# Optimization experiments

Hardware: AMD Instinct MI355X
Metric: run time of the kernel (lower is better)

Reference implementation:

```python
import jax, jax.numpy as jnp
import numpy as np
import math

HIDDEN = 1024
N_HEAD = 16
D_K = HIDDEN // N_HEAD

def setup_inputs() -> dict:
    key = jax.random.key(0)
    ks = jax.random.split(key, 6)
    B, T = 2, 2048
    x = jax.random.normal(ks[0], (B, T, HIDDEN), dtype=jnp.float32)
    mask = jax.random.randint(ks[1], (B, 1, 1, T), 0, 2, dtype=jnp.int32)
    s = 1.0 / math.sqrt(HIDDEN)
    W_qkv = jax.random.normal(ks[2], (HIDDEN, 3 * HIDDEN), dtype=jnp.float32) * s
    b_qkv = jnp.zeros((3 * HIDDEN,), dtype=jnp.float32)
    W_out = jax.random.normal(ks[3], (HIDDEN, HIDDEN), dtype=jnp.float32) * s
    b_out = jnp.zeros((HIDDEN,), dtype=jnp.float32)
    return {"x": x, "mask": mask, "W_qkv": W_qkv, "b_qkv": b_qkv, "W_out": W_out, "b_out": b_out}

def reference(x, mask, W_qkv, b_qkv, W_out, b_out):
    B, T, H = x.shape
    qkv = x @ W_qkv + b_qkv  # [B,T,3H]
    q, k, v = jnp.split(qkv, 3, axis=-1)
    # [B,T,H] -> [B,nh,T,dk]
    def split_heads(t):
        return t.reshape(B, T, N_HEAD, D_K).transpose(0, 2, 1, 3)
    q, k, v = split_heads(q), split_heads(k), split_heads(v)
    scores = jnp.einsum('bhqd,bhkd->bhqk', q, k) / math.sqrt(D_K)
    scores = jnp.where(mask == 0, jnp.float32(-1e9), scores)
    attn = jax.nn.softmax(scores, axis=-1)
    out = jnp.einsum('bhqk,bhkd->bhqd', attn, v)
    out = out.transpose(0, 2, 1, 3).reshape(B, T, H)
    return out @ W_out + b_out
```

## Files before the change

### kernel.cpp

```cpp
#include <hip/hip_runtime.h>
#include <stdint.h>

typedef unsigned short u16;
typedef unsigned int u32;
typedef short bf16x8 __attribute__((ext_vector_type(8)));
typedef float f32x4 __attribute__((ext_vector_type(4)));

#define MFMA16(a, b, c) __builtin_amdgcn_mfma_f32_16x16x32_bf16((a), (b), (c), 0, 0, 0)
#define BAR()                              \
  do {                                     \
    __builtin_amdgcn_sched_barrier(0);     \
    __builtin_amdgcn_s_barrier();          \
    __builtin_amdgcn_sched_barrier(0);     \
  } while (0)

__device__ __forceinline__ u16 f2bf(float f) {
  union { float f; u32 u; } v; v.f = f;
  u32 u = v.u;
  u32 r = (u + 0x7FFFu + ((u >> 16) & 1u)) >> 16;
  return (u16)r;
}
__device__ __forceinline__ float bf2f(u16 h) {
  union { u32 u; float f; } v; v.u = ((u32)h) << 16;
  return v.f;
}
__device__ __forceinline__ u32 cvtpk_bf16(float lo, float hi) {
  u32 r;
  asm("v_cvt_pk_bf16_f32 %0, %1, %2" : "=v"(r) : "v"(lo), "v"(hi));
  return r;
}

__device__ __forceinline__ void gload_lds16(const void* g, void* l) {
  __builtin_amdgcn_global_load_lds(
      (const __attribute__((address_space(1))) unsigned int*)g,
      (__attribute__((address_space(3))) unsigned int*)l,
      16, 0, 0);
}

__global__ __launch_bounds__(256) void transpose_weights(
    const float* __restrict__ Wqkv, u16* __restrict__ WtQ,
    const float* __restrict__ Wout, u16* __restrict__ WtO) {
  __shared__ u16 t[32][33];
  int id = blockIdx.x;
  const float* src;
  u16* dst;
  int C, bx, by;
  if (id < 3072) {
    src = Wqkv; dst = WtQ; C = 3072;
    bx = (id % 96) * 32; by = (id / 96) * 32;
  } else {
    id -= 3072;
    src = Wout; dst = WtO; C = 1024;
    bx = (id % 32) * 32; by = (id / 32) * 32;
  }
  const int R = 1024;
  const int tx = threadIdx.x & 31, ty = threadIdx.x >> 5;
#pragma unroll
  for (int i = 0; i < 32; i += 8)
    t[ty + i][tx] = f2bf(src[(size_t)(by + ty + i) * C + bx + tx]);
  __syncthreads();
#pragma unroll
  for (int i = 0; i < 32; i += 8)
    dst[(size_t)(bx + ty + i) * R + by + tx] = t[tx][ty + i];
}

__global__ __launch_bounds__(512) void mask_compact(
    const int* __restrict__ mask, int* __restrict__ idx, int* __restrict__ cnt) {
  const int b = blockIdx.x;
  const int tid = threadIdx.x;
  const int lane = tid & 63, wave = tid >> 6;
  __shared__ int wtot[8];
  int m[4], c = 0;
#pragma unroll
  for (int j = 0; j < 4; ++j) {
    m[j] = (mask[b * 2048 + tid * 4 + j] != 0);
    c += m[j];
  }
  int pfx = c;
#pragma unroll
  for (int sh = 1; sh < 64; sh <<= 1) {
    int v = __shfl_up(pfx, sh);
    if (lane >= sh) pfx += v;
  }
  if (lane == 63) wtot[wave] = pfx;
  int epfx = pfx - c;
  __syncthreads();
  int wbase = 0, total = 0;
#pragma unroll
  for (int w = 0; w < 8; ++w) {
    int v = wtot[w];
    if (w < wave) wbase += v;
    total += v;
  }
  int pos = b * 2048 + wbase + epfx;
#pragma unroll
  for (int j = 0; j < 4; ++j)
    if (m[j]) idx[pos++] = tid * 4 + j;
  for (int i = total + tid; i < 2048; i += 512) idx[b * 2048 + i] = 0;
  if (tid == 0) cnt[b] = total;
}

__global__ __launch_bounds__(256) void gemm_a32_bf16(
    const float* __restrict__ A, const u16* __restrict__ Bt,
    const float* __restrict__ bias, u16* __restrict__ Cout,
    int M, int N, int K) {
  __shared__ __align__(16) u16 As[128 * 64];
  __shared__ __align__(16) u16 Bs[2][128 * 64];
  const int tid = threadIdx.x;
  const int lane = tid & 63;
  const int wave = tid >> 6;
  const int nwg = gridDim.x;
  const int id = blockIdx.x;
  const int sw = (id & 7) * (nwg >> 3) + (id >> 3);
  const int nx = N >> 7;
  const int m0 = (sw / nx) * 128;
  const int n0 = (sw % nx) * 128;
  const int wm = (wave >> 1) * 64;
  const int wn = (wave & 1) * 64;

  f32x4 acc[4][4] = {};
  const char* Bbase = (const char*)Bt;
  float4 fa[4], fb[4];

#define A32_ISSUE_B(ktile, buf)                                                \
  _Pragma("unroll") for (int i = 0; i < 4; ++i) {                              \
    int flat = wave * 1024 + lane * 16 + i * 4096;                             \
    int row = flat >> 7;                                                       \
    int cb = flat & 127;                                                       \
    int scb = cb ^ ((row & 7) << 4);                                           \
    gload_lds16(Bbase + ((size_t)(n0 + row) * K + (ktile)) * 2 + scb,          \
                (char*)&Bs[buf][0] + flat);                                    \
  }

#define A32_LOAD_A(ktile)                                                      \
  _Pragma("unroll") for (int i = 0; i < 4; ++i) {                              \
    int flat = wave * 1024 + lane * 16 + i * 4096;                             \
    int row = flat >> 7;                                                       \
    int cb = flat & 127;                                                       \
    const float* ax = A + (size_t)(m0 + row) * K + (ktile) + (cb >> 1);        \
    fa[i] = *(const float4*)ax;                                                \
    fb[i] = *(const float4*)(ax + 4);                                          \
  }

#define A32_CVT()                                                              \
  _Pragma("unroll") for (int i = 0; i < 4; ++i) {                              \
    int flat = wave * 1024 + lane * 16 + i * 4096;                             \
    int row = flat >> 7;                                                       \
    int cb = flat & 127;                                                       \
    union { u32 w[4]; bf16x8 v; } o;                                           \
    o.w[0] = cvtpk_bf16(fa[i].x, fa[i].y);                                     \
    o.w[1] = cvtpk_bf16(fa[i].z, fa[i].w);                                     \
    o.w[2] = cvtpk_bf16(fb[i].x, fb[i].y);                                     \
    o.w[3] = cvtpk_bf16(fb[i].z, fb[i].w);                                     \
    *(bf16x8*)((char*)&As[0] + row * 128 + (cb ^ ((row & 7) << 4))) = o.v;     \
  }

  A32_ISSUE_B(0, 0);
  A32_LOAD_A(0);
  A32_CVT();
  asm volatile("s_waitcnt lgkmcnt(0)" ::: "memory");
  BAR();

  const int nsteps = K >> 6;
  for (int t = 0; t < nsteps; ++t) {
    if (t < nsteps - 1) {
      A32_ISSUE_B((t << 6) + 64, (t & 1) ^ 1);
      A32_LOAD_A((t << 6) + 64);
    }
    __builtin_amdgcn_sched_barrier(0);
#pragma unroll
    for (int ks = 0; ks < 2; ++ks) {
      const int col = (lane >> 4) * 8 + ks * 32;
      bf16x8 af[4], bfr[4];
#pragma unroll
      for (int mt = 0; mt < 4; ++mt) {
        int row = wm + mt * 16 + (lane & 15);
        af[mt] = *(const bf16x8*)((const char*)&As[0] + row * 128 +
                                  ((col * 2) ^ ((row & 7) << 4)));
      }
#pragma unroll
      for (int nt = 0; nt < 4; ++nt) {
        int row = wn + nt * 16 + (lane & 15);
        bfr[nt] = *(const bf16x8*)((const char*)&Bs[t & 1][0] + row * 128 +
                                   ((col * 2) ^ ((row & 7) << 4)));
      }
#pragma unroll
      for (int mt = 0; mt < 4; ++mt)
#pragma unroll
        for (int nt = 0; nt < 4; ++nt)
          acc[mt][nt] = MFMA16(af[mt], bfr[nt], acc[mt][nt]);
    }
    __builtin_amdgcn_sched_barrier(0);
    if (t < nsteps - 1) {
      BAR();
      A32_CVT();
      asm volatile("s_waitcnt lgkmcnt(0)" ::: "memory");
      BAR();
    }
  }
#undef A32_ISSUE_B
#undef A32_LOAD_A
#undef A32_CVT

  float bv[4];
#pragma unroll
  for (int nt = 0; nt < 4; ++nt)
    bv[nt] = bias[n0 + wn + nt * 16 + (lane & 15)];
#pragma unroll
  for (int mt = 0; mt < 4; ++mt)
#pragma unroll
    for (int nt = 0; nt < 4; ++nt)
#pragma unroll
      for (int r = 0; r < 4; ++r) {
        int m = m0 + wm + mt * 16 + (lane >> 4) * 4 + r;
        int n = n0 + wn + nt * 16 + (lane & 15);
        Cout[(size_t)m * N + n] = f2bf(acc[mt][nt][r] + bv[nt]);
      }
}

template <bool OUT_BF16>
__global__ __launch_bounds__(256) void gemm_bf16(
    const u16* __restrict__ A, const u16* __restrict__ Bt,
    const float* __restrict__ bias, void* __restrict__ Cout,
    int M, int N, int K) {
  __shared__ __align__(16) u16 As[2][128 * 64];
  __shared__ __align__(16) u16 Bs[2][128 * 64];
  const int tid = threadIdx.x;
  const int lane = tid & 63;
  const int wave = tid >> 6;
  const int nwg = gridDim.x;
  const int id = blockIdx.x;
  const int sw = (id & 7) * (nwg >> 3) + (id >> 3);
  const int nx = N >> 7;
  const int m0 = (sw / nx) * 128;
  const int n0 = (sw % nx) * 128;
  const int wm = (wave >> 1) * 64;
  const int wn = (wave & 1) * 64;

  f32x4 acc[4][4] = {};

  const char* Abase = (const char*)A;
  const char* Bbase = (const char*)Bt;

#define STAGE_AB(ktile, buf)                                                   \
  _Pragma("unroll") for (int i = 0; i < 4; ++i) {                              \
    int flat = wave * 1024 + lane * 16 + i * 4096;                             \
    int row = flat >> 7;                                                       \
    int cb = flat & 127;                                                       \
    int scb = cb ^ ((row & 7) << 4);                                           \
    gload_lds16(Abase + ((size_t)(m0 + row) * K + (ktile)) * 2 + scb,          \
                (char*)&As[buf][0] + flat);                                    \
    gload_lds16(Bbase + ((size_t)(n0 + row) * K + (ktile)) * 2 + scb,          \
                (char*)&Bs[buf][0] + flat);                                    \
  }

  STAGE_AB(0, 0);

  const int nsteps = K >> 6;
  for (int t = 0; t < nsteps; ++t) {
    asm volatile("s_waitcnt vmcnt(0)" ::: "memory");
    BAR();
    if (t < nsteps - 1) STAGE_AB((t << 6) + 64, (t & 1) ^ 1);
#pragma unroll
    for (int ks = 0; ks < 2; ++ks) {
      const int col = (lane >> 4) * 8 + ks * 32;
      bf16x8 af[4], bfr[4];
#pragma unroll
      for (int mt = 0; mt < 4; ++mt) {
        int row = wm + mt * 16 + (lane & 15);
        af[mt] = *(const bf16x8*)((const char*)&As[t & 1][0] + row * 128 +
                                  ((col * 2) ^ ((row & 7) << 4)));
      }
#pragma unroll
      for (int nt = 0; nt < 4; ++nt) {
        int row = wn + nt * 16 + (lane & 15);
        bfr[nt] = *(const bf16x8*)((const char*)&Bs[t & 1][0] + row * 128 +
                                   ((col * 2) ^ ((row & 7) << 4)));
      }
#pragma unroll
      for (int mt = 0; mt < 4; ++mt)
#pragma unroll
        for (int nt = 0; nt < 4; ++nt)
          acc[mt][nt] = MFMA16(af[mt], bfr[nt], acc[mt][nt]);
    }
  }
#undef STAGE_AB

  float bv[4];
#pragma unroll
  for (int nt = 0; nt < 4; ++nt)
    bv[nt] = bias[n0 + wn + nt * 16 + (lane & 15)];
#pragma unroll
  for (int mt = 0; mt < 4; ++mt)
#pragma unroll
    for (int nt = 0; nt < 4; ++nt)
#pragma unroll
      for (int r = 0; r < 4; ++r) {
        int m = m0 + wm + mt * 16 + (lane >> 4) * 4 + r;
        int n = n0 + wn + nt * 16 + (lane & 15);
        float v = acc[mt][nt][r] + bv[nt];
        if (OUT_BF16)
          ((u16*)Cout)[(size_t)m * N + n] = f2bf(v);
        else
          ((float*)Cout)[(size_t)m * N + n] = v;
      }
}

#define T_SEQ 2048
#define ROWQKV 3072
#define SCL 0.180336880f

template <bool SPLIT>
__global__ __launch_bounds__(512) void attn_fwd(
    const u16* __restrict__ qkv, const int* __restrict__ idx,
    const int* __restrict__ cnt, u16* __restrict__ outp,
    float* __restrict__ Ml) {
  __shared__ __align__(16) u16 Ks[2][2][64 * 64];
  __shared__ __align__(16) u16 Vt[2][2][64 * 64];
  __shared__ __align__(16) u32 lut[256 * 4];

  const int tid = threadIdx.x;
  const int lane = tid & 63;
  const int wave = tid >> 6;
  const int r15 = lane & 15;
  const int g = lane >> 4;
  const int id = blockIdx.x;
  const int hz = ((id >> 6) << 3) | (id & 7);
  const int qb = (id >> 3) & 7;
  const int h = SPLIT ? (hz >> 2) : (hz >> 1);
  const int z = SPLIT ? (hz & 3) : (hz & 1);
  const int split = SPLIT ? (z >> 1) : 0;
  const int b = SPLIT ? (z & 1) : z;
  const int q0 = qb * 256 + wave * 32;
  const size_t rowb = (size_t)b * T_SEQ;
  const int* idxb = idx + b * 2048;
  const int count = cnt[b];
  const int ntot = (count + 127) >> 7;
  const int nth = (ntot + 1) >> 1;
  const int t0 = (SPLIT && split) ? nth : 0;
  const int nt2 = SPLIT ? (split ? ntot - nth : nth) : ntot;

  const int Lk = wave * 1024 + lane * 16;
  const int krow = Lk >> 7;
  const int kscb = (Lk & 127) ^ ((krow & 7) << 4);
  const int kprow = ((krow >> 4) & 1) * 32 + ((krow >> 2) & 3) * 8 +
                    (krow >> 5) * 4 + (krow & 3);
  const int vkey = tid >> 3;
  const int vd0 = (tid & 7) * 8;

  for (int i = tid; i < 256; i += 512) {
    union { u32 w[4]; bf16x8 v; } e;
#pragma unroll
    for (int j = 0; j < 4; ++j)
      e.w[j] = (((i >> (2 * j)) & 1) ? 0x3F80u : 0u) |
               (((i >> (2 * j + 1)) & 1) ? 0x3F800000u : 0u);
    *(bf16x8*)((char*)lut + i * 16) = e.v;
  }

  bf16x8 aq[2][2];
#pragma unroll
  for (int mt = 0; mt < 2; ++mt)
#pragma unroll
    for (int ks = 0; ks < 2; ++ks) {
      bf16x8 t = *(const bf16x8*)(qkv +
          (rowb + q0 + mt * 16 + r15) * ROWQKV + h * 64 + g * 8 + ks * 32);
#pragma unroll
      for (int j = 0; j < 8; ++j) t[j] = (short)f2bf(bf2f((u16)t[j]) * SCL);
      aq[mt][ks] = t;
    }

  f32x4 accO[2][4] = {};
  f32x4 ssum[2] = {};
  bf16x8 vr0, vr1;
  int ik0, ik1, iv0, iv1;

#define LOAD_IDX(ct)                                                           \
  {                                                                            \
    ik0 = idxb[(ct) * 128 + kprow];                                            \
    ik1 = idxb[(ct) * 128 + 64 + kprow];                                       \
    iv0 = idxb[(ct) * 128 + vkey];                                             \
    iv1 = idxb[(ct) * 128 + 64 + vkey];                                        \
  }

#define ISSUE_K2R(buf)                                                         \
  {                                                                            \
    gload_lds16((const char*)qkv +                                             \
                    ((rowb + ik0) * ROWQKV + 1024 + h * 64) * 2 + kscb,        \
                (char*)&Ks[buf][0][0] + wave * 1024);                          \
    gload_lds16((const char*)qkv +                                             \
                    ((rowb + ik1) * ROWQKV + 1024 + h * 64) * 2 + kscb,        \
                (char*)&Ks[buf][1][0] + wave * 1024);                          \
  }

#define LOAD_V2R()                                                             \
  {                                                                            \
    vr0 = *(const bf16x8*)(qkv + (rowb + iv0) * ROWQKV + 2048 + h * 64 + vd0); \
    vr1 = *(const bf16x8*)(qkv + (rowb + iv1) * ROWQKV + 2048 + h * 64 + vd0); \
  }

#define WRITE_V2(buf, ct)                                                      \
  {                                                                            \
    if ((ct) * 128 + vkey >= count) {                                          \
      bf16x8 zz = {};                                                          \
      vr0 = zz;                                                                \
    }                                                                          \
    if ((ct) * 128 + 64 + vkey >= count) {                                     \
      bf16x8 zz = {};                                                          \
      vr1 = zz;                                                                \
    }                                                                          \
    _Pragma("unroll") for (int j = 0; j < 8; ++j) {                            \
      int row = vd0 + j;                                                       \
      int sv = ((row ^ (row >> 3)) & 7) << 4;                                  \
      *(u16*)((char*)&Vt[buf][0][0] + row * 128 + ((vkey * 2) ^ sv)) =         \
          (u16)vr0[j];                                                         \
      *(u16*)((char*)&Vt[buf][1][0] + row * 128 + ((vkey * 2) ^ sv)) =         \
          (u16)vr1[j];                                                         \
    }                                                                          \
  }

#define COMPUTE_HALF(H, ct)                                                    \
  {                                                                            \
    f32x4 s[2][4] = {};                                                        \
    _Pragma("unroll") for (int ks = 0; ks < 2; ++ks) {                         \
      bf16x8 bk[4];                                                            \
      _Pragma("unroll") for (int nt = 0; nt < 4; ++nt) {                       \
        int row = nt * 16 + r15;                                               \
        int cb = (g * 8 + ks * 32) * 2;                                        \
        bk[nt] = *(const bf16x8*)((const char*)&Ks[cur][H][0] + row * 128 +    \
                                  (cb ^ ((row & 7) << 4)));                    \
      }                                                                        \
      _Pragma("unroll") for (int mt = 0; mt < 2; ++mt)                         \
        _Pragma("unroll") for (int nt = 0; nt < 4; ++nt)                       \
          s[mt][nt] = MFMA16(bk[nt], aq[mt][ks], s[mt][nt]);                   \
    }                                                                          \
    u32 pk[2][4][2];                                                           \
    _Pragma("unroll") for (int mt = 0; mt < 2; ++mt)                           \
      _Pragma("unroll") for (int nt = 0; nt < 4; ++nt) {                       \
        float e0 = exp2f(s[mt][nt][0]);                                        \
        float e1 = exp2f(s[mt][nt][1]);                                        \
        float e2 = exp2f(s[mt][nt][2]);                                        \
        float e3 = exp2f(s[mt][nt][3]);                                        \
        pk[mt][nt][0] = cvtpk_bf16(e0, e1);                                    \
        pk[mt][nt][1] = cvtpk_bf16(e2, e3);                                    \
      }                                                                        \
    __builtin_amdgcn_s_setprio(1);                                             \
    _Pragma("unroll") for (int ks = 0; ks < 2; ++ks) {                         \
      const int col = g * 8 + ks * 32;                                         \
      bf16x8 bv[4];                                                            \
      _Pragma("unroll") for (int nt = 0; nt < 4; ++nt) {                       \
        int row = nt * 16 + r15;                                               \
        int sv = ((row ^ (row >> 3)) & 7) << 4;                                \
        bv[nt] = *(const bf16x8*)((const char*)&Vt[cur][H][0] + row * 128 +    \
                                  ((col * 2) ^ sv));                           \
      }                                                                        \
      int rbase = count - ((ct) * 128 + (H) * 64 + ks * 32 + g * 8);           \
      int rr = rbase < 0 ? 0 : (rbase > 8 ? 8 : rbase);                        \
      u32 lb = (1u << rr) - 1u;                                                \
      bf16x8 mf = *(const bf16x8*)((const char*)lut + lb * 16);                \
      _Pragma("unroll") for (int mt = 0; mt < 2; ++mt) {                       \
        union { u32 w[4]; bf16x8 v; } ap;                                      \
        ap.w[0] = pk[mt][ks][0];                                               \
        ap.w[1] = pk[mt][ks][1];                                               \
        ap.w[2] = pk[mt][2 + ks][0];                                           \
        ap.w[3] = pk[mt][2 + ks][1];                                           \
        _Pragma("unroll") for (int nt = 0; nt < 4; ++nt)                       \
          accO[mt][nt] = MFMA16(ap.v, bv[nt], accO[mt][nt]);                   \
        ssum[mt] = MFMA16(ap.v, mf, ssum[mt]);                                 \
      }                                                                        \
    }                                                                          \
    __builtin_amdgcn_s_setprio(0);                                             \
  }

  if (nt2 > 0) {
    LOAD_IDX(t0);
    ISSUE_K2R(0);
    LOAD_V2R();
    if (nt2 > 1) LOAD_IDX(t0 + 1);
    __syncthreads();
    WRITE_V2(0, t0);
    asm volatile("s_waitcnt lgkmcnt(0)" ::: "memory");
    BAR();

    int cur = 0;
    for (int t = 0; t < nt2; ++t) {
      const int ct = t0 + t;
      if (t < nt2 - 1) {
        ISSUE_K2R(cur ^ 1);
        LOAD_V2R();
        if (t < nt2 - 2) LOAD_IDX(ct + 2);
      }

      COMPUTE_HALF(0, ct);
      COMPUTE_HALF(1, ct);

      if (t < nt2 - 1) {
        asm volatile("s_waitcnt vmcnt(0)" ::: "memory");
        WRITE_V2(cur ^ 1, ct + 1);
        asm volatile("s_waitcnt lgkmcnt(0)" ::: "memory");
        BAR();
        cur ^= 1;
      }
    }
  }

  if (SPLIT) {
    u16* po = outp + (size_t)split * T_SEQ * 2 * 1024;
#pragma unroll
    for (int mt = 0; mt < 2; ++mt) {
#pragma unroll
      for (int r = 0; r < 4; ++r) {
        int q = q0 + mt * 16 + g * 4 + r;
#pragma unroll
        for (int nt = 0; nt < 4; ++nt)
          po[(rowb + q) * 1024 + h * 64 + nt * 16 + r15] = f2bf(accO[mt][nt][r]);
      }
      if (r15 == 0) {
        int idxm = ((split * 2 + b) * 16 + h) * T_SEQ + q0 + mt * 16 + g * 4;
        *(f32x4*)(Ml + idxm) = ssum[mt];
      }
    }
  } else {
#pragma unroll
    for (int mt = 0; mt < 2; ++mt)
#pragma unroll
      for (int r = 0; r < 4; ++r) {
        float inv = 1.f / ssum[mt][r];
        int q = q0 + mt * 16 + g * 4 + r;
#pragma unroll
        for (int nt = 0; nt < 4; ++nt)
          outp[(rowb + q) * 1024 + h * 64 + nt * 16 + r15] =
              f2bf(accO[mt][nt][r] * inv);
      }
  }
#undef LOAD_IDX
#undef ISSUE_K2R
#undef LOAD_V2R
#undef WRITE_V2
#undef COMPUTE_HALF
}

__global__ __launch_bounds__(256) void attn_combine(
    const u16* __restrict__ part, const float* __restrict__ Ml,
    u16* __restrict__ att) {
  int idx = blockIdx.x * 256 + threadIdx.x;
  int row = idx >> 7;
  int c8 = idx & 127;
  int col = c8 * 8;
  int h = c8 >> 3;
  int b = row >> 11, q = row & 2047;
  float l0 = Ml[(b * 16 + h) * T_SEQ + q];
  float l1 = Ml[((2 + b) * 16 + h) * T_SEQ + q];
  float inv = 1.f / (l0 + l1);
  bf16x8 o0 = *(const bf16x8*)(part + (size_t)row * 1024 + col);
  bf16x8 o1 = *(const bf16x8*)(part + (size_t)T_SEQ * 2 * 1024 +
                               (size_t)row * 1024 + col);
  bf16x8 o;
#pragma unroll
  for (int j = 0; j < 8; ++j)
    o[j] = (short)f2bf((bf2f((u16)o0[j]) + bf2f((u16)o1[j])) * inv);
  *(bf16x8*)(att + (size_t)row * 1024 + col) = o;
}

extern "C" void kernel_launch(void* const* d_in, const int* in_sizes, int n_in,
                              void* d_out, int out_size, void* d_ws, size_t ws_size,
                              hipStream_t stream) {
  const float* x = (const float*)d_in[0];
  const int* mask = (const int*)d_in[1];
  const float* Wqkv = (const float*)d_in[2];
  const float* bqkv = (const float*)d_in[3];
  const float* Wout = (const float*)d_in[4];
  const float* bout = (const float*)d_in[5];
  float* out = (float*)d_out;

  const int B = 2, T = 2048, H = 1024, M = B * T;

  u16* qkv = (u16*)d_ws;
  u16* att = qkv + (size_t)M * 3 * H;
  u16* WtQ = att + (size_t)M * H;
  u16* WtO = WtQ + (size_t)3 * H * H;
  u16* part = WtO + (size_t)H * H;
  float* Ml = (float*)(part + (size_t)2 * M * H);
  int* idxb = (int*)(Ml + (size_t)2 * 131072);
  int* cntb = idxb + B * T;

  const size_t need = ((size_t)M * 3 * H + (size_t)M * H + (size_t)3 * H * H +
                       (size_t)H * H + (size_t)2 * M * H) * 2 +
                      (size_t)2 * 131072 * 4 + (size_t)(B * T + 8) * 4;
  const bool split = ws_size >= need;

  transpose_weights<<<3072 + 1024, 256, 0, stream>>>(Wqkv, WtQ, Wout, WtO);
  mask_compact<<<B, 512, 0, stream>>>(mask, idxb, cntb);
  gemm_a32_bf16<<<(3 * H / 128) * (M / 128), 256, 0, stream>>>(x, WtQ, bqkv, qkv, M, 3 * H, H);
  if (split) {
    attn_fwd<true><<<512, 512, 0, stream>>>(qkv, idxb, cntb, part, Ml);
    attn_combine<<<(M * H / 8 + 255) / 256, 256, 0, stream>>>(part, Ml, att);
  } else {
    attn_fwd<false><<<256, 512, 0, stream>>>(qkv, idxb, cntb, att, Ml);
  }
  gemm_bf16<false><<<(H / 128) * (M / 128), 256, 0, stream>>>(att, WtO, bout, out, M, H, H);
}
```

Measured before the change: 117.7 us.

## Split attention KV range four ways and single-buffer K/V shared memory

Generalizes the split-KV attention to a templated NSPLIT, launching 1024 blocks with four key-range splits when workspace allows, and generalizes the combine kernel to sum NSPLIT partials. The K/V LDS tiles go from double-buffered to single-buffered: loads for the next tile are issued after compute behind an extra barrier. This halves shared memory per block to raise occupancy and adds parallelism over the masked key range. In exchange it loses load/compute overlap within a block and adds more partial-output traffic in the combine step.

```diff
diff --git a/kernel.cpp b/kernel.cpp
--- a/kernel.cpp
+++ b/kernel.cpp
@@ -310,13 +310,13 @@
 #define ROWQKV 3072
 #define SCL 0.180336880f
 
-template <bool SPLIT>
+template <int NSPLIT>
 __global__ __launch_bounds__(512) void attn_fwd(
     const u16* __restrict__ qkv, const int* __restrict__ idx,
     const int* __restrict__ cnt, u16* __restrict__ outp,
     float* __restrict__ Ml) {
-  __shared__ __align__(16) u16 Ks[2][2][64 * 64];
-  __shared__ __align__(16) u16 Vt[2][2][64 * 64];
+  __shared__ __align__(16) u16 Ks[2][64 * 64];
+  __shared__ __align__(16) u16 Vt[2][64 * 64];
   __shared__ __align__(16) u32 lut[256 * 4];
 
   const int tid = threadIdx.x;
@@ -327,18 +327,19 @@
   const int id = blockIdx.x;
   const int hz = ((id >> 6) << 3) | (id & 7);
   const int qb = (id >> 3) & 7;
-  const int h = SPLIT ? (hz >> 2) : (hz >> 1);
-  const int z = SPLIT ? (hz & 3) : (hz & 1);
-  const int split = SPLIT ? (z >> 1) : 0;
-  const int b = SPLIT ? (z & 1) : z;
+  int h, split, b;
+  if (NSPLIT == 4) { h = hz >> 3; split = (hz & 7) >> 1; b = hz & 1; }
+  else if (NSPLIT == 2) { h = hz >> 2; split = (hz & 3) >> 1; b = hz & 1; }
+  else { h = hz >> 1; split = 0; b = hz & 1; }
   const int q0 = qb * 256 + wave * 32;
   const size_t rowb = (size_t)b * T_SEQ;
   const int* idxb = idx + b * 2048;
   const int count = cnt[b];
   const int ntot = (count + 127) >> 7;
-  const int nth = (ntot + 1) >> 1;
-  const int t0 = (SPLIT && split) ? nth : 0;
-  const int nt2 = SPLIT ? (split ? ntot - nth : nth) : ntot;
+  const int nth = (ntot + NSPLIT - 1) / NSPLIT;
+  const int t0 = split * nth;
+  int rem = ntot - t0;
+  const int nt2 = rem < 0 ? 0 : (rem < nth ? rem : nth);
 
   const int Lk = wave * 1024 + lane * 16;
   const int krow = Lk >> 7;
@@ -382,14 +383,14 @@
     iv1 = idxb[(ct) * 128 + 64 + vkey];                                        \
   }
 
-#define ISSUE_K2R(buf)                                                         \
+#define ISSUE_K2R()                                                            \
   {                                                                            \
     gload_lds16((const char*)qkv +                                             \
                     ((rowb + ik0) * ROWQKV + 1024 + h * 64) * 2 + kscb,        \
-                (char*)&Ks[buf][0][0] + wave * 1024);                          \
+                (char*)&Ks[0][0] + wave * 1024);                               \
     gload_lds16((const char*)qkv +                                             \
                     ((rowb + ik1) * ROWQKV + 1024 + h * 64) * 2 + kscb,        \
-                (char*)&Ks[buf][1][0] + wave * 1024);                          \
+                (char*)&Ks[1][0] + wave * 1024);                               \
   }
 
 #define LOAD_V2R()                                                             \
@@ -398,7 +399,7 @@
     vr1 = *(const bf16x8*)(qkv + (rowb + iv1) * ROWQKV + 2048 + h * 64 + vd0); \
   }
 
-#define WRITE_V2(buf, ct)                                                      \
+#define WRITE_V2(ct)                                                           \
   {                                                                            \
     if ((ct) * 128 + vkey >= count) {                                          \
       bf16x8 zz = {};                                                          \
@@ -411,10 +412,8 @@
     _Pragma("unroll") for (int j = 0; j < 8; ++j) {                            \
       int row = vd0 + j;                                                       \
       int sv = ((row ^ (row >> 3)) & 7) << 4;                                  \
-      *(u16*)((char*)&Vt[buf][0][0] + row * 128 + ((vkey * 2) ^ sv)) =         \
-          (u16)vr0[j];                                                         \
-      *(u16*)((char*)&Vt[buf][1][0] + row * 128 + ((vkey * 2) ^ sv)) =         \
-          (u16)vr1[j];                                                         \
+      *(u16*)((char*)&Vt[0][0] + row * 128 + ((vkey * 2) ^ sv)) = (u16)vr0[j]; \
+      *(u16*)((char*)&Vt[1][0] + row * 128 + ((vkey * 2) ^ sv)) = (u16)vr1[j]; \
     }                                                                          \
   }
 
@@ -426,7 +425,7 @@
       _Pragma("unroll") for (int nt = 0; nt < 4; ++nt) {                       \
         int row = nt * 16 + r15;                                               \
         int cb = (g * 8 + ks * 32) * 2;                                        \
-        bk[nt] = *(const bf16x8*)((const char*)&Ks[cur][H][0] + row * 128 +    \
+        bk[nt] = *(const bf16x8*)((const char*)&Ks[H][0] + row * 128 +         \
                                   (cb ^ ((row & 7) << 4)));                    \
       }                                                                        \
       _Pragma("unroll") for (int mt = 0; mt < 2; ++mt)                         \
@@ -450,7 +449,7 @@
       _Pragma("unroll") for (int nt = 0; nt < 4; ++nt) {                       \
         int row = nt * 16 + r15;                                               \
         int sv = ((row ^ (row >> 3)) & 7) << 4;                                \
-        bv[nt] = *(const bf16x8*)((const char*)&Vt[cur][H][0] + row * 128 +    \
+        bv[nt] = *(const bf16x8*)((const char*)&Vt[H][0] + row * 128 +         \
                                   ((col * 2) ^ sv));                           \
       }                                                                        \
       int rbase = count - ((ct) * 128 + (H) * 64 + ks * 32 + g * 8);           \
@@ -473,37 +472,33 @@
 
   if (nt2 > 0) {
     LOAD_IDX(t0);
-    ISSUE_K2R(0);
+    ISSUE_K2R();
     LOAD_V2R();
     if (nt2 > 1) LOAD_IDX(t0 + 1);
     __syncthreads();
-    WRITE_V2(0, t0);
+    WRITE_V2(t0);
     asm volatile("s_waitcnt lgkmcnt(0)" ::: "memory");
     BAR();
 
-    int cur = 0;
     for (int t = 0; t < nt2; ++t) {
       const int ct = t0 + t;
+      COMPUTE_HALF(0, ct);
+      COMPUTE_HALF(1, ct);
+
       if (t < nt2 - 1) {
-        ISSUE_K2R(cur ^ 1);
+        BAR();
+        ISSUE_K2R();
         LOAD_V2R();
         if (t < nt2 - 2) LOAD_IDX(ct + 2);
-      }
-
-      COMPUTE_HALF(0, ct);
-      COMPUTE_HALF(1, ct);
-
-      if (t < nt2 - 1) {
         asm volatile("s_waitcnt vmcnt(0)" ::: "memory");
-        WRITE_V2(cur ^ 1, ct + 1);
+        WRITE_V2(ct + 1);
         asm volatile("s_waitcnt lgkmcnt(0)" ::: "memory");
         BAR();
-        cur ^= 1;
       }
     }
   }
 
-  if (SPLIT) {
+  if (NSPLIT > 1) {
     u16* po = outp + (size_t)split * T_SEQ * 2 * 1024;
 #pragma unroll
     for (int mt = 0; mt < 2; ++mt) {
@@ -539,6 +534,7 @@
 #undef COMPUTE_HALF
 }
 
+template <int NSPLIT>
 __global__ __launch_bounds__(256) void attn_combine(
     const u16* __restrict__ part, const float* __restrict__ Ml,
     u16* __restrict__ att) {
@@ -548,17 +544,24 @@
   int col = c8 * 8;
   int h = c8 >> 3;
   int b = row >> 11, q = row & 2047;
-  float l0 = Ml[(b * 16 + h) * T_SEQ + q];
-  float l1 = Ml[((2 + b) * 16 + h) * T_SEQ + q];
-  float inv = 1.f / (l0 + l1);
-  bf16x8 o0 = *(const bf16x8*)(part + (size_t)row * 1024 + col);
-  bf16x8 o1 = *(const bf16x8*)(part + (size_t)T_SEQ * 2 * 1024 +
-                               (size_t)row * 1024 + col);
-  bf16x8 o;
-#pragma unroll
-  for (int j = 0; j < 8; ++j)
-    o[j] = (short)f2bf((bf2f((u16)o0[j]) + bf2f((u16)o1[j])) * inv);
-  *(bf16x8*)(att + (size_t)row * 1024 + col) = o;
+  float l = 0.f;
+#pragma unroll
+  for (int s = 0; s < NSPLIT; ++s)
+    l += Ml[((s * 2 + b) * 16 + h) * T_SEQ + q];
+  float inv = 1.f / l;
+  float acc[8] = {};
+#pragma unroll
+  for (int s = 0; s < NSPLIT; ++s) {
+    bf16x8 o = *(const bf16x8*)(part + (size_t)s * T_SEQ * 2 * 1024 +
+                                (size_t)row * 1024 + col);
+#pragma unroll
+    for (int j = 0; j < 8; ++j) acc[j] += bf2f((u16)o[j]);
+  }
+  union { u32 w[4]; bf16x8 v; } o;
+#pragma unroll
+  for (int j = 0; j < 4; ++j)
+    o.w[j] = cvtpk_bf16(acc[2 * j] * inv, acc[2 * j + 1] * inv);
+  *(bf16x8*)(att + (size_t)row * 1024 + col) = o.v;
 }
 
 extern "C" void kernel_launch(void* const* d_in, const int* in_sizes, int n_in,
@@ -578,24 +581,28 @@
   u16* att = qkv + (size_t)M * 3 * H;
   u16* WtQ = att + (size_t)M * H;
   u16* WtO = WtQ + (size_t)3 * H * H;
-  u16* part = WtO + (size_t)H * H;
-  float* Ml = (float*)(part + (size_t)2 * M * H);
-  int* idxb = (int*)(Ml + (size_t)2 * 131072);
+  float* Ml = (float*)(WtO + (size_t)H * H);
+  int* idxb = (int*)(Ml + (size_t)4 * 65536);
   int* cntb = idxb + B * T;
-
-  const size_t need = ((size_t)M * 3 * H + (size_t)M * H + (size_t)3 * H * H +
-                       (size_t)H * H + (size_t)2 * M * H) * 2 +
-                      (size_t)2 * 131072 * 4 + (size_t)(B * T + 8) * 4;
-  const bool split = ws_size >= need;
+  u16* part = (u16*)(cntb + 8);
+
+  const size_t fixed = ((size_t)M * 3 * H + (size_t)M * H + (size_t)3 * H * H +
+                        (size_t)H * H) * 2 +
+                       (size_t)4 * 65536 * 4 + (size_t)(B * T + 8) * 4;
+  const size_t need4 = fixed + (size_t)4 * M * H * 2;
+  const size_t need2 = fixed + (size_t)2 * M * H * 2;
 
   transpose_weights<<<3072 + 1024, 256, 0, stream>>>(Wqkv, WtQ, Wout, WtO);
   mask_compact<<<B, 512, 0, stream>>>(mask, idxb, cntb);
   gemm_a32_bf16<<<(3 * H / 128) * (M / 128), 256, 0, stream>>>(x, WtQ, bqkv, qkv, M, 3 * H, H);
-  if (split) {
-    attn_fwd<true><<<512, 512, 0, stream>>>(qkv, idxb, cntb, part, Ml);
-    attn_combine<<<(M * H / 8 + 255) / 256, 256, 0, stream>>>(part, Ml, att);
+  if (ws_size >= need4) {
+    attn_fwd<4><<<1024, 512, 0, stream>>>(qkv, idxb, cntb, part, Ml);
+    attn_combine<4><<<(M * H / 8 + 255) / 256, 256, 0, stream>>>(part, Ml, att);
+  } else if (ws_size >= need2) {
+    attn_fwd<2><<<512, 512, 0, stream>>>(qkv, idxb, cntb, part, Ml);
+    attn_combine<2><<<(M * H / 8 + 255) / 256, 256, 0, stream>>>(part, Ml, att);
   } else {
-    attn_fwd<false><<<256, 512, 0, stream>>>(qkv, idxb, cntb, att, Ml);
+    attn_fwd<1><<<256, 512, 0, stream>>>(qkv, idxb, cntb, att, Ml);
   }
   gemm_bf16<false><<<(H / 128) * (M / 128), 256, 0, stream>>>(att, WtO, bout, out, M, H, H);
 }
```

New measurement: 132.6 us. +12.7%, slower.
